# Kernel optimization log

Measured on AMD Instinct MI355X. Metric: run time of the kernel, lower is better.

The kernel has to match this reference:

```python
import jax, jax.numpy as jnp
import numpy as np

N = 300000   # nodes
E = 1500000  # edges
G = 30000    # graphs
R = 3        # relations
EMB = 32
HID = 64
OUT = 2


def rgcn_conv(x, src, dst, edge_type, W, root, bias, num_nodes):
    """PyG RGCNConv: out_i = x_i @ root + bias + sum_r mean_{j in N_r(i)} x_j @ W_r."""
    out = x @ root + bias
    for r in range(W.shape[0]):
        xr = x @ W[r]                                  # [N, out] transform once per relation
        mask = (edge_type == r).astype(x.dtype)        # [E]
        msg = xr[src] * mask[:, None]                  # gather + mask  [E, out]
        agg = jax.ops.segment_sum(msg, dst, num_segments=num_nodes)
        cnt = jax.ops.segment_sum(mask, dst, num_segments=num_nodes)
        out = out + agg / jnp.maximum(cnt, 1.0)[:, None]
    return out


def global_mean_pool(x, batch, num_graphs):
    s = jax.ops.segment_sum(x, batch, num_segments=num_graphs)
    c = jax.ops.segment_sum(jnp.ones((x.shape[0],), x.dtype), batch, num_segments=num_graphs)
    return s / jnp.maximum(c, 1.0)[:, None]


def setup_inputs() -> dict:
    key = jax.random.key(0)
    ks = jax.random.split(key, 16)
    def glorot(k, shape):
        fan_in, fan_out = shape[-2], shape[-1]
        lim = np.sqrt(6.0 / (fan_in + fan_out)).astype(np.float32)
        return jax.random.uniform(k, shape, jnp.float32, -lim, lim)
    return {
        "sid": jax.random.randint(ks[0], (N,), 0, 26),
        "cid": jax.random.randint(ks[1], (N,), 0, 10),
        "pid": jax.random.randint(ks[2], (N,), 0, 128),
        "edge_index": jax.random.randint(ks[3], (2, E), 0, N),
        "edge_type": jax.random.randint(ks[4], (E,), 0, R),
        "batch": jnp.sort(jax.random.randint(ks[5], (N,), 0, G)),
        "num_graphs": G,
        "shape_emb": jax.random.normal(ks[6], (26, EMB), jnp.float32),
        "col_emb": jax.random.normal(ks[7], (10, EMB), jnp.float32),
        "pos_emb": jax.random.normal(ks[8], (128, EMB), jnp.float32),
        "W1": glorot(ks[9], (R, EMB, HID)),
        "root1": glorot(ks[10], (EMB, HID)),
        "b1": jnp.zeros((HID,), jnp.float32),
        "W2": glorot(ks[11], (R, HID, HID)),
        "root2": glorot(ks[12], (HID, HID)),
        "b2": jnp.zeros((HID,), jnp.float32),
        "lin_W": glorot(ks[13], (HID, OUT)),
        "lin_b": jnp.zeros((OUT,), jnp.float32),
    }


def reference(sid, cid, pid, edge_index, edge_type, batch, num_graphs,
              shape_emb, col_emb, pos_emb,
              W1, root1, b1, W2, root2, b2, lin_W, lin_b):
    num_nodes = sid.shape[0]
    src, dst = edge_index[0], edge_index[1]
    x = shape_emb[sid] + col_emb[cid] + pos_emb[pid]          # [N, 32]
    x = jax.nn.relu(rgcn_conv(x, src, dst, edge_type, W1, root1, b1, num_nodes))
    x = jax.nn.relu(rgcn_conv(x, src, dst, edge_type, W2, root2, b2, num_nodes))
    g = global_mean_pool(x, batch, num_graphs)                 # [G, 64]
    return g @ lin_W + lin_b                                   # [G, 2]
```

## Files before the change

### kernel.cpp

```cpp
#include <hip/hip_runtime.h>
#include <hip/hip_bf16.h>

#define NREL 3
#define EMB 32
#define HID 64

typedef __attribute__((ext_vector_type(8))) short short8_t;
typedef __attribute__((ext_vector_type(4))) short short4_t;
typedef __attribute__((ext_vector_type(4))) float f32x4;

__device__ inline short f2bf(float v) {
  __hip_bfloat16 b = __float2bfloat16(v);
  short s;
  __builtin_memcpy(&s, &b, 2);
  return s;
}
__device__ inline float bf2f(short s) {
  __hip_bfloat16 b;
  __builtin_memcpy(&b, &s, 2);
  return __bfloat162float(b);
}
__device__ inline void split8(const float* v, short8_t* h, short8_t* l) {
#pragma unroll
  for (int i = 0; i < 8; i++) {
    short hh = f2bf(v[i]);
    (*h)[i] = hh;
    (*l)[i] = f2bf(v[i] - bf2f(hh));
  }
}

__global__ __launch_bounds__(256) void prep_k(
    const int* __restrict__ sid, const int* __restrict__ cid, const int* __restrict__ pid,
    const float* __restrict__ se, const float* __restrict__ ce, const float* __restrict__ pe,
    short* __restrict__ xh, short* __restrict__ xl,
    const int* __restrict__ dst, const int* __restrict__ et, int* __restrict__ icnt,
    const float* __restrict__ root1, const float* __restrict__ W1,
    const float* __restrict__ root2, const float* __restrict__ W2,
    short* __restrict__ w1h, short* __restrict__ w1l,
    short* __restrict__ w2h, short* __restrict__ w2l, int N, int E) {
  int i = blockIdx.x * 256 + threadIdx.x;
  if (i < N * 8) {
    int n = i >> 3, cg = i & 7;
    const float4 a = *(const float4*)&se[sid[n] * EMB + cg * 4];
    const float4 b = *(const float4*)&ce[cid[n] * EMB + cg * 4];
    const float4 c = *(const float4*)&pe[pid[n] * EMB + cg * 4];
    float v[4];
    v[0] = a.x + b.x + c.x; v[1] = a.y + b.y + c.y;
    v[2] = a.z + b.z + c.z; v[3] = a.w + b.w + c.w;
    short4_t h, l;
#pragma unroll
    for (int j = 0; j < 4; j++) {
      short hh = f2bf(v[j]);
      h[j] = hh;
      l[j] = f2bf(v[j] - bf2f(hh));
    }
    *(short4_t*)&xh[(size_t)n * EMB + cg * 4] = h;
    *(short4_t*)&xl[(size_t)n * EMB + cg * 4] = l;
  }
  if (i < E) atomicAdd(&icnt[et[i] * N + dst[i]], 1);
  if (i < 64 * 128) {
    int k = i >> 6, n = i & 63;
    float v = (k < EMB) ? root1[k * 64 + n] : W1[(k - EMB) * 64 + n];
    short h = f2bf(v);
    w1h[n * 128 + k] = h;
    w1l[n * 128 + k] = f2bf(v - bf2f(h));
  }
  if (i < 64 * 256) {
    int k = i >> 6, n = i & 63;
    float v = (k < HID) ? root2[k * 64 + n] : W2[(k - HID) * 64 + n];
    short h = f2bf(v);
    w2h[n * 256 + k] = h;
    w2l[n * 256 + k] = f2bf(v - bf2f(h));
  }
}

__global__ __launch_bounds__(256) void scan1_k(const int* __restrict__ icnt,
                                               int* __restrict__ psum, int M) {
  int base = blockIdx.x * 1024 + threadIdx.x * 4;
  int s = 0;
#pragma unroll
  for (int j = 0; j < 4; j++) {
    int i = base + j;
    if (i < M) s += icnt[i];
  }
  __shared__ int tmp[256];
  tmp[threadIdx.x] = s;
  __syncthreads();
  for (int off = 128; off > 0; off >>= 1) {
    if (threadIdx.x < off) tmp[threadIdx.x] += tmp[threadIdx.x + off];
    __syncthreads();
  }
  if (threadIdx.x == 0) psum[blockIdx.x] = tmp[0];
}

__global__ __launch_bounds__(256) void scan2_k(int* __restrict__ psum, int P) {
  __shared__ int tmp[256];
  __shared__ int carry_s;
  if (threadIdx.x == 0) carry_s = 0;
  __syncthreads();
  for (int base = 0; base < P; base += 256) {
    int i = base + threadIdx.x;
    int v = (i < P) ? psum[i] : 0;
    tmp[threadIdx.x] = v;
    __syncthreads();
    for (int off = 1; off < 256; off <<= 1) {
      int u = (threadIdx.x >= off) ? tmp[threadIdx.x - off] : 0;
      __syncthreads();
      tmp[threadIdx.x] += u;
      __syncthreads();
    }
    int carry = carry_s;
    if (i < P) psum[i] = carry + tmp[threadIdx.x] - v;
    __syncthreads();
    if (threadIdx.x == 0) carry_s = carry + tmp[255];
    __syncthreads();
  }
}

__global__ __launch_bounds__(256) void scan3_k(const int* __restrict__ icnt,
                                               const int* __restrict__ psum,
                                               int* __restrict__ offs, int M) {
  int base = blockIdx.x * 1024 + threadIdx.x * 4;
  int v[4];
  int s = 0;
#pragma unroll
  for (int j = 0; j < 4; j++) {
    int i = base + j;
    v[j] = (i < M) ? icnt[i] : 0;
    s += v[j];
  }
  __shared__ int tmp[256];
  tmp[threadIdx.x] = s;
  __syncthreads();
  for (int off = 1; off < 256; off <<= 1) {
    int u = (threadIdx.x >= off) ? tmp[threadIdx.x - off] : 0;
    __syncthreads();
    tmp[threadIdx.x] += u;
    __syncthreads();
  }
  int run = psum[blockIdx.x] + tmp[threadIdx.x] - s;
#pragma unroll
  for (int j = 0; j < 4; j++) {
    int i = base + j;
    if (i < M) {
      offs[i] = run;
      run += v[j];
    }
  }
}

__global__ __launch_bounds__(256) void scatter_k(const int* __restrict__ src,
                                                 const int* __restrict__ dst,
                                                 const int* __restrict__ et,
                                                 const int* __restrict__ offs,
                                                 int* __restrict__ cursor,
                                                 int* __restrict__ nbr,
                                                 int* __restrict__ csr, int E, int N) {
  int e = blockIdx.x * 256 + threadIdx.x;
  if (e >= E) return;
  int idx = et[e] * N + dst[e];
  int j = atomicAdd(&cursor[idx], 1);
  int s = src[e];
  if (j < 4) nbr[(size_t)idx * 4 + j] = s;
  else csr[offs[idx] + j] = s;
}

__global__ __launch_bounds__(256) void l1fused_k(
    const short* __restrict__ xh, const short* __restrict__ xl,
    const int* __restrict__ offs, const int* __restrict__ icnt,
    const int* __restrict__ nbr, const int* __restrict__ csr,
    const short* __restrict__ wth, const short* __restrict__ wtl,
    const float* __restrict__ bias, short* __restrict__ h1h, short* __restrict__ h1l, int N) {
  __shared__ __align__(16) short lws[64][16][8];
  __shared__ __align__(16) short gh_s[192][4][8];
  __shared__ __align__(16) short gl_s[192][4][8];
  __shared__ __align__(16) int4 mid_s[192];
  __shared__ int mlen_s[192];
  __shared__ int mbeg_s[192];

  const int t = threadIdx.x;
  const int lane = t & 63, w = t >> 6;
  const int m_ = lane & 15, q = lane >> 4;
  const int n0b = blockIdx.x * 64;

  int node_c = n0b + w * 16 + m_;
  if (node_c >= N) node_c = N - 1;
  short8_t ah0 = *(const short8_t*)&xh[(size_t)node_c * EMB + q * 8];
  short8_t al0 = *(const short8_t*)&xl[(size_t)node_c * EMB + q * 8];
#pragma unroll
  for (int i = 0; i < 4; i++) {
    int chi = t + 256 * i;
    int row = chi >> 4, c = chi & 15;
    short8_t wv = *(const short8_t*)&wth[(size_t)row * 128 + c * 8];
    *(short8_t*)&lws[row][c ^ (row & 7)][0] = wv;
  }
  if (t < 192) {
    int r = t >> 6, nl = t & 63;
    int n_ = n0b + nl;
    if (n_ >= N) n_ = N - 1;
    int idx = r * N + n_;
    mid_s[t] = *(const int4*)&nbr[(size_t)idx * 4];
    mlen_s[t] = icnt[idx];
    mbeg_s[t] = offs[idx];
  }
  __syncthreads();

  {
    int tslot[3], tq[3], tlen[3], tbeg[3];
    int4 tid4[3];
#pragma unroll
    for (int k = 0; k < 3; k++) {
      int tau = t + 256 * k;
      tslot[k] = tau >> 2;
      tq[k] = tau & 3;
      tid4[k] = mid_s[tslot[k]];
      tlen[k] = mlen_s[tslot[k]];
      tbeg[k] = mbeg_s[tslot[k]];
    }
    short8_t v0[3], v1[3], v2[3], v3[3];
#pragma unroll
    for (int k = 0; k < 3; k++) {
      int nself = n0b + (tslot[k] & 63);
      if (nself >= N) nself = N - 1;
      int g0 = (0 < tlen[k]) ? tid4[k].x : nself;
      int g1 = (1 < tlen[k]) ? tid4[k].y : nself;
      int g2 = (2 < tlen[k]) ? tid4[k].z : nself;
      int g3 = (3 < tlen[k]) ? tid4[k].w : nself;
      size_t co = (size_t)tq[k] * 8;
      v0[k] = *(const short8_t*)&xh[(size_t)g0 * EMB + co];
      v1[k] = *(const short8_t*)&xh[(size_t)g1 * EMB + co];
      v2[k] = *(const short8_t*)&xh[(size_t)g2 * EMB + co];
      v3[k] = *(const short8_t*)&xh[(size_t)g3 * EMB + co];
    }
#pragma unroll
    for (int k = 0; k < 3; k++) {
      float a[8];
      float k0 = (0 < tlen[k]) ? 1.f : 0.f;
      float k1 = (1 < tlen[k]) ? 1.f : 0.f;
      float k2 = (2 < tlen[k]) ? 1.f : 0.f;
      float k3 = (3 < tlen[k]) ? 1.f : 0.f;
#pragma unroll
      for (int i = 0; i < 8; i++)
        a[i] = k0 * bf2f(v0[k][i]) + k1 * bf2f(v1[k][i]) + k2 * bf2f(v2[k][i]) +
               k3 * bf2f(v3[k][i]);
      for (int j = 4; j < tlen[k]; j++) {
        short8_t u = *(const short8_t*)&xh[(size_t)csr[tbeg[k] + j] * EMB + tq[k] * 8];
#pragma unroll
        for (int i = 0; i < 8; i++) a[i] += bf2f(u[i]);
      }
      float inv = 1.f / fmaxf((float)tlen[k], 1.f);
#pragma unroll
      for (int i = 0; i < 8; i++) a[i] *= inv;
      short8_t hi, lo;
      split8(a, &hi, &lo);
      int qs = tq[k] ^ (tslot[k] & 3);
      *(short8_t*)&gh_s[tslot[k]][qs][0] = hi;
      *(short8_t*)&gl_s[tslot[k]][qs][0] = lo;
    }
  }
  __syncthreads();

  f32x4 acc[4];
#pragma unroll
  for (int i = 0; i < 4; i++) acc[i] = (f32x4){0.f, 0.f, 0.f, 0.f};
  short8_t ahv[4], alv[4];
#pragma unroll
  for (int g = 0; g < 4; g++) {
    if (g == 0) {
      ahv[0] = ah0;
      alv[0] = al0;
    } else {
      int slot = (g - 1) * 64 + w * 16 + m_;
      int qs = q ^ (slot & 3);
      ahv[g] = *(const short8_t*)&gh_s[slot][qs][0];
      alv[g] = *(const short8_t*)&gl_s[slot][qs][0];
    }
#pragma unroll
    for (int tt = 0; tt < 4; tt++) {
      int row = 16 * tt + m_;
      int cs = (g * 4 + q) ^ (row & 7);
      short8_t bh = *(const short8_t*)&lws[row][cs][0];
      acc[tt] = __builtin_amdgcn_mfma_f32_16x16x32_bf16(ahv[g], bh, acc[tt], 0, 0, 0);
      acc[tt] = __builtin_amdgcn_mfma_f32_16x16x32_bf16(alv[g], bh, acc[tt], 0, 0, 0);
    }
  }
  __syncthreads();

#pragma unroll
  for (int i = 0; i < 4; i++) {
    int chi = t + 256 * i;
    int row = chi >> 4, c = chi & 15;
    short8_t wv = *(const short8_t*)&wtl[(size_t)row * 128 + c * 8];
    *(short8_t*)&lws[row][c ^ (row & 7)][0] = wv;
  }
  __syncthreads();

#pragma unroll
  for (int g = 0; g < 4; g++) {
#pragma unroll
    for (int tt = 0; tt < 4; tt++) {
      int row = 16 * tt + m_;
      int cs = (g * 4 + q) ^ (row & 7);
      short8_t bl = *(const short8_t*)&lws[row][cs][0];
      acc[tt] = __builtin_amdgcn_mfma_f32_16x16x32_bf16(ahv[g], bl, acc[tt], 0, 0, 0);
    }
  }
#pragma unroll
  for (int tt = 0; tt < 4; tt++) {
    float bia = bias[16 * tt + m_];
#pragma unroll
    for (int reg = 0; reg < 4; reg++) {
      int node = n0b + w * 16 + q * 4 + reg;
      if (node < N) {
        float val = fmaxf(acc[tt][reg] + bia, 0.f);
        short hh = f2bf(val);
        h1h[(size_t)node * HID + 16 * tt + m_] = hh;
        h1l[(size_t)node * HID + 16 * tt + m_] = f2bf(val - bf2f(hh));
      }
    }
  }
}

__global__ __launch_bounds__(256) void l2fused_k(
    const short* __restrict__ h1h, const short* __restrict__ h1l,
    const int* __restrict__ offs, const int* __restrict__ icnt,
    const int* __restrict__ nbr, const int* __restrict__ csr,
    const short* __restrict__ wth, const short* __restrict__ wtl,
    const float* __restrict__ bias, const float* __restrict__ linW,
    const int* __restrict__ batch, float* __restrict__ gs, float* __restrict__ gc, int N) {
  __shared__ __align__(16) short lws[64][16][8];
  __shared__ __align__(16) short gh_s[192][4][8];
  __shared__ __align__(16) short gl_s[192][4][8];
  __shared__ __align__(16) int4 mid_s[192];
  __shared__ int mlen_s[192];
  __shared__ int mbeg_s[192];

  const int t = threadIdx.x;
  const int lane = t & 63, w = t >> 6;
  const int m_ = lane & 15, q = lane >> 4;
  const int n0b = blockIdx.x * 64;

  int node_c = n0b + w * 16 + m_;
  if (node_c >= N) node_c = N - 1;
  short8_t ash[2], asl[2];
#pragma unroll
  for (int s_ = 0; s_ < 2; s_++) {
    ash[s_] = *(const short8_t*)&h1h[(size_t)node_c * HID + s_ * 32 + q * 8];
    asl[s_] = *(const short8_t*)&h1l[(size_t)node_c * HID + s_ * 32 + q * 8];
  }
#pragma unroll
  for (int i = 0; i < 4; i++) {
    int chi = t + 256 * i;
    int row = chi >> 4, c = chi & 15;
    int g = c >> 2, qq = c & 3;
    short8_t wv = *(const short8_t*)&wth[(size_t)row * 256 + g * 64 + 0 * 32 + qq * 8];
    *(short8_t*)&lws[row][c ^ (row & 7)][0] = wv;
  }
  if (t < 192) {
    int r = t >> 6, nl = t & 63;
    int n_ = n0b + nl;
    if (n_ >= N) n_ = N - 1;
    int idx = r * N + n_;
    mid_s[t] = *(const int4*)&nbr[(size_t)idx * 4];
    mlen_s[t] = icnt[idx];
    mbeg_s[t] = offs[idx];
  }
  __syncthreads();

  f32x4 acc[4];
#pragma unroll
  for (int i = 0; i < 4; i++) acc[i] = (f32x4){0.f, 0.f, 0.f, 0.f};

#pragma unroll
  for (int s_ = 0; s_ < 2; s_++) {
    if (s_ == 1) {
#pragma unroll
      for (int i = 0; i < 4; i++) {
        int chi = t + 256 * i;
        int row = chi >> 4, c = chi & 15;
        int g = c >> 2, qq = c & 3;
        short8_t wv = *(const short8_t*)&wth[(size_t)row * 256 + g * 64 + 32 + qq * 8];
        *(short8_t*)&lws[row][c ^ (row & 7)][0] = wv;
      }
    }
    int tslot[3], tq[3], tlen[3], tbeg[3];
    int4 tid4[3];
#pragma unroll
    for (int k = 0; k < 3; k++) {
      int tau = t + 256 * k;
      tslot[k] = tau >> 2;
      tq[k] = tau & 3;
      tid4[k] = mid_s[tslot[k]];
      tlen[k] = mlen_s[tslot[k]];
      tbeg[k] = mbeg_s[tslot[k]];
    }
    short8_t v0[3], v1[3], v2[3], v3[3];
#pragma unroll
    for (int k = 0; k < 3; k++) {
      int nself = n0b + (tslot[k] & 63);
      if (nself >= N) nself = N - 1;
      int g0 = (0 < tlen[k]) ? tid4[k].x : nself;
      int g1 = (1 < tlen[k]) ? tid4[k].y : nself;
      int g2 = (2 < tlen[k]) ? tid4[k].z : nself;
      int g3 = (3 < tlen[k]) ? tid4[k].w : nself;
      size_t co = (size_t)s_ * 32 + tq[k] * 8;
      v0[k] = *(const short8_t*)&h1h[(size_t)g0 * HID + co];
      v1[k] = *(const short8_t*)&h1h[(size_t)g1 * HID + co];
      v2[k] = *(const short8_t*)&h1h[(size_t)g2 * HID + co];
      v3[k] = *(const short8_t*)&h1h[(size_t)g3 * HID + co];
    }
#pragma unroll
    for (int k = 0; k < 3; k++) {
      float a[8];
      float k0 = (0 < tlen[k]) ? 1.f : 0.f;
      float k1 = (1 < tlen[k]) ? 1.f : 0.f;
      float k2 = (2 < tlen[k]) ? 1.f : 0.f;
      float k3 = (3 < tlen[k]) ? 1.f : 0.f;
#pragma unroll
      for (int i = 0; i < 8; i++)
        a[i] = k0 * bf2f(v0[k][i]) + k1 * bf2f(v1[k][i]) + k2 * bf2f(v2[k][i]) +
               k3 * bf2f(v3[k][i]);
      for (int j = 4; j < tlen[k]; j++) {
        short8_t u =
            *(const short8_t*)&h1h[(size_t)csr[tbeg[k] + j] * HID + s_ * 32 + tq[k] * 8];
#pragma unroll
        for (int i = 0; i < 8; i++) a[i] += bf2f(u[i]);
      }
      float inv = 1.f / fmaxf((float)tlen[k], 1.f);
#pragma unroll
      for (int i = 0; i < 8; i++) a[i] *= inv;
      short8_t hi, lo;
      split8(a, &hi, &lo);
      int qs = tq[k] ^ (tslot[k] & 3);
      *(short8_t*)&gh_s[tslot[k]][qs][0] = hi;
      *(short8_t*)&gl_s[tslot[k]][qs][0] = lo;
    }
    __syncthreads();

    short8_t ahv[4], alv[4];
#pragma unroll
    for (int g = 0; g < 4; g++) {
      if (g == 0) {
        ahv[0] = ash[s_];
        alv[0] = asl[s_];
      } else {
        int slot = (g - 1) * 64 + w * 16 + m_;
        int qs = q ^ (slot & 3);
        ahv[g] = *(const short8_t*)&gh_s[slot][qs][0];
        alv[g] = *(const short8_t*)&gl_s[slot][qs][0];
      }
#pragma unroll
      for (int tt = 0; tt < 4; tt++) {
        int row = 16 * tt + m_;
        int cs = (g * 4 + q) ^ (row & 7);
        short8_t bh = *(const short8_t*)&lws[row][cs][0];
        acc[tt] = __builtin_amdgcn_mfma_f32_16x16x32_bf16(ahv[g], bh, acc[tt], 0, 0, 0);
        acc[tt] = __builtin_amdgcn_mfma_f32_16x16x32_bf16(alv[g], bh, acc[tt], 0, 0, 0);
      }
    }
    __syncthreads();

#pragma unroll
    for (int i = 0; i < 4; i++) {
      int chi = t + 256 * i;
      int row = chi >> 4, c = chi & 15;
      int g = c >> 2, qq = c & 3;
      short8_t wv = *(const short8_t*)&wtl[(size_t)row * 256 + g * 64 + s_ * 32 + qq * 8];
      *(short8_t*)&lws[row][c ^ (row & 7)][0] = wv;
    }
    __syncthreads();

#pragma unroll
    for (int g = 0; g < 4; g++) {
#pragma unroll
      for (int tt = 0; tt < 4; tt++) {
        int row = 16 * tt + m_;
        int cs = (g * 4 + q) ^ (row & 7);
        short8_t bl = *(const short8_t*)&lws[row][cs][0];
        acc[tt] = __builtin_amdgcn_mfma_f32_16x16x32_bf16(ahv[g], bl, acc[tt], 0, 0, 0);
      }
    }
    if (s_ == 0) __syncthreads();
  }

  float bia[4], lw0[4], lw1[4];
#pragma unroll
  for (int tt = 0; tt < 4; tt++) {
    int col = 16 * tt + m_;
    bia[tt] = bias[col];
    lw0[tt] = linW[col * 2 + 0];
    lw1[tt] = linW[col * 2 + 1];
  }
#pragma unroll
  for (int reg = 0; reg < 4; reg++) {
    int node = n0b + w * 16 + q * 4 + reg;
    float p0 = 0.f, p1 = 0.f;
#pragma unroll
    for (int tt = 0; tt < 4; tt++) {
      float v = fmaxf(acc[tt][reg] + bia[tt], 0.f);
      p0 += v * lw0[tt];
      p1 += v * lw1[tt];
    }
#pragma unroll
    for (int o = 1; o < 16; o <<= 1) {
      p0 += __shfl_xor(p0, o, 64);
      p1 += __shfl_xor(p1, o, 64);
    }
    if (m_ == 0 && node < N) {
      int g = batch[node];
      atomicAdd(&gs[g * 2 + 0], p0);
      atomicAdd(&gs[g * 2 + 1], p1);
      atomicAdd(&gc[g], 1.0f);
    }
  }
}

__global__ __launch_bounds__(256) void final_k(const float* __restrict__ gs,
                                               const float* __restrict__ gc,
                                               const float* __restrict__ linb,
                                               float* __restrict__ out, int G) {
  int i = blockIdx.x * 256 + threadIdx.x;
  if (i >= G * 2) return;
  int g = i >> 1, o = i & 1;
  out[i] = gs[i] / fmaxf(gc[g], 1.0f) + linb[o];
}

extern "C" void kernel_launch(void* const* d_in, const int* in_sizes, int n_in,
                              void* d_out, int out_size, void* d_ws, size_t ws_size,
                              hipStream_t stream) {
  const int* sid = (const int*)d_in[0];
  const int* cid = (const int*)d_in[1];
  const int* pid = (const int*)d_in[2];
  const int* ei = (const int*)d_in[3];
  const int* et = (const int*)d_in[4];
  const int* batch = (const int*)d_in[5];
  const float* se = (const float*)d_in[7];
  const float* ce = (const float*)d_in[8];
  const float* pe = (const float*)d_in[9];
  const float* W1 = (const float*)d_in[10];
  const float* root1 = (const float*)d_in[11];
  const float* b1 = (const float*)d_in[12];
  const float* W2 = (const float*)d_in[13];
  const float* root2 = (const float*)d_in[14];
  const float* b2 = (const float*)d_in[15];
  const float* linW = (const float*)d_in[16];
  const float* linb = (const float*)d_in[17];
  float* out = (float*)d_out;

  const int N = in_sizes[0];
  const int E = in_sizes[4];
  const int G = out_size / 2;
  const int* src = ei;
  const int* dst = ei + E;
  const int M = N * NREL;
  const int P = (M + 1023) / 1024;

  char* w = (char*)d_ws;
  short* h1h = (short*)w;  w += (size_t)N * HID * sizeof(short);
  short* h1l = (short*)w;  w += (size_t)N * HID * sizeof(short);
  short* xh = (short*)w;   w += (size_t)N * EMB * sizeof(short);
  short* xl = (short*)w;   w += (size_t)N * EMB * sizeof(short);
  float* gs = (float*)w;   w += (size_t)G * 2 * sizeof(float);
  float* gc = (float*)w;   w += (size_t)G * sizeof(float);
  int* icnt = (int*)w;     w += (size_t)M * sizeof(int);
  int* cursor = (int*)w;   w += (size_t)M * sizeof(int);
  int* offs = (int*)w;     w += (size_t)M * sizeof(int);
  int* nbr = (int*)w;      w += (size_t)M * 4 * sizeof(int);
  int* csr = (int*)w;      w += (size_t)E * sizeof(int);
  short* w1h = (short*)w;  w += (size_t)64 * 128 * sizeof(short);
  short* w1l = (short*)w;  w += (size_t)64 * 128 * sizeof(short);
  short* w2h = (short*)w;  w += (size_t)64 * 256 * sizeof(short);
  short* w2l = (short*)w;  w += (size_t)64 * 256 * sizeof(short);
  int* psum = (int*)w;     w += (size_t)P * sizeof(int);
  if ((size_t)(w - (char*)d_ws) > ws_size) return;

  hipMemsetAsync(icnt, 0, (size_t)2 * M * sizeof(int), stream);
  hipMemsetAsync(gs, 0, (size_t)G * 3 * sizeof(float), stream);

  int prep_n = N * 8;
  if (prep_n < E) prep_n = E;
  if (prep_n < 64 * 256) prep_n = 64 * 256;
  prep_k<<<(prep_n + 255) / 256, 256, 0, stream>>>(sid, cid, pid, se, ce, pe, xh, xl, dst, et,
                                                   icnt, root1, W1, root2, W2, w1h, w1l, w2h,
                                                   w2l, N, E);
  scan1_k<<<P, 256, 0, stream>>>(icnt, psum, M);
  scan2_k<<<1, 256, 0, stream>>>(psum, P);
  scan3_k<<<P, 256, 0, stream>>>(icnt, psum, offs, M);
  scatter_k<<<(E + 255) / 256, 256, 0, stream>>>(src, dst, et, offs, cursor, nbr, csr, E, N);

  int blocks = (N + 63) / 64;
  l1fused_k<<<blocks, 256, 0, stream>>>(xh, xl, offs, icnt, nbr, csr, w1h, w1l, b1, h1h, h1l,
                                        N);
  l2fused_k<<<blocks, 256, 0, stream>>>(h1h, h1l, offs, icnt, nbr, csr, w2h, w2l, b2, linW,
                                        batch, gs, gc, N);
  final_k<<<(G * 2 + 255) / 256, 256, 0, stream>>>(gs, gc, linb, out, G);
}
```

Baseline: 468.3 us.

## Replace per-(relation,node) CSR with per-block bucketed packed edge lists

Edges are now bucketed by destination block of 64 nodes, with dst-local index, relation and source packed into one 32-bit word. This replaces the three-pass per-(relation,node) scan, the cursor array and the inline-4 neighbour layout with a single small scan over block counts. The fused layer kernels then scatter-add gathered features into shared-memory fp32 accumulators using LDS atomics, and divide by counts before the MFMA stage. This cuts preprocessing memory traffic and kernel launches and balances edge work across threads, at the cost of many shared-memory float atomics and a 19-bit limit on source node ids.

```diff
diff --git a/kernel.cpp b/kernel.cpp
--- a/kernel.cpp
+++ b/kernel.cpp
@@ -33,7 +33,7 @@
     const int* __restrict__ sid, const int* __restrict__ cid, const int* __restrict__ pid,
     const float* __restrict__ se, const float* __restrict__ ce, const float* __restrict__ pe,
     short* __restrict__ xh, short* __restrict__ xl,
-    const int* __restrict__ dst, const int* __restrict__ et, int* __restrict__ icnt,
+    const int* __restrict__ dst, int* __restrict__ bcnt,
     const float* __restrict__ root1, const float* __restrict__ W1,
     const float* __restrict__ root2, const float* __restrict__ W2,
     short* __restrict__ w1h, short* __restrict__ w1l,
@@ -57,7 +57,7 @@
     *(short4_t*)&xh[(size_t)n * EMB + cg * 4] = h;
     *(short4_t*)&xl[(size_t)n * EMB + cg * 4] = l;
   }
-  if (i < E) atomicAdd(&icnt[et[i] * N + dst[i]], 1);
+  if (i < E) atomicAdd(&bcnt[dst[i] >> 6], 1);
   if (i < 64 * 128) {
     int k = i >> 6, n = i & 63;
     float v = (k < EMB) ? root1[k * 64 + n] : W1[(k - EMB) * 64 + n];
@@ -74,33 +74,16 @@
   }
 }
 
-__global__ __launch_bounds__(256) void scan1_k(const int* __restrict__ icnt,
-                                               int* __restrict__ psum, int M) {
-  int base = blockIdx.x * 1024 + threadIdx.x * 4;
-  int s = 0;
-#pragma unroll
-  for (int j = 0; j < 4; j++) {
-    int i = base + j;
-    if (i < M) s += icnt[i];
-  }
-  __shared__ int tmp[256];
-  tmp[threadIdx.x] = s;
-  __syncthreads();
-  for (int off = 128; off > 0; off >>= 1) {
-    if (threadIdx.x < off) tmp[threadIdx.x] += tmp[threadIdx.x + off];
-    __syncthreads();
-  }
-  if (threadIdx.x == 0) psum[blockIdx.x] = tmp[0];
-}
-
-__global__ __launch_bounds__(256) void scan2_k(int* __restrict__ psum, int P) {
+__global__ __launch_bounds__(256) void bscan_k(const int* __restrict__ bcnt,
+                                               int* __restrict__ boffs,
+                                               int* __restrict__ bcur, int NBk) {
   __shared__ int tmp[256];
   __shared__ int carry_s;
   if (threadIdx.x == 0) carry_s = 0;
   __syncthreads();
-  for (int base = 0; base < P; base += 256) {
+  for (int base = 0; base < NBk; base += 256) {
     int i = base + threadIdx.x;
-    int v = (i < P) ? psum[i] : 0;
+    int v = (i < NBk) ? bcnt[i] : 0;
     tmp[threadIdx.x] = v;
     __syncthreads();
     for (int off = 1; off < 256; off <<= 1) {
@@ -110,73 +93,38 @@
       __syncthreads();
     }
     int carry = carry_s;
-    if (i < P) psum[i] = carry + tmp[threadIdx.x] - v;
+    if (i < NBk) {
+      int ex = carry + tmp[threadIdx.x] - v;
+      boffs[i] = ex;
+      bcur[i] = ex;
+    }
     __syncthreads();
     if (threadIdx.x == 0) carry_s = carry + tmp[255];
     __syncthreads();
   }
-}
-
-__global__ __launch_bounds__(256) void scan3_k(const int* __restrict__ icnt,
-                                               const int* __restrict__ psum,
-                                               int* __restrict__ offs, int M) {
-  int base = blockIdx.x * 1024 + threadIdx.x * 4;
-  int v[4];
-  int s = 0;
-#pragma unroll
-  for (int j = 0; j < 4; j++) {
-    int i = base + j;
-    v[j] = (i < M) ? icnt[i] : 0;
-    s += v[j];
-  }
-  __shared__ int tmp[256];
-  tmp[threadIdx.x] = s;
-  __syncthreads();
-  for (int off = 1; off < 256; off <<= 1) {
-    int u = (threadIdx.x >= off) ? tmp[threadIdx.x - off] : 0;
-    __syncthreads();
-    tmp[threadIdx.x] += u;
-    __syncthreads();
-  }
-  int run = psum[blockIdx.x] + tmp[threadIdx.x] - s;
-#pragma unroll
-  for (int j = 0; j < 4; j++) {
-    int i = base + j;
-    if (i < M) {
-      offs[i] = run;
-      run += v[j];
-    }
-  }
-}
-
-__global__ __launch_bounds__(256) void scatter_k(const int* __restrict__ src,
-                                                 const int* __restrict__ dst,
-                                                 const int* __restrict__ et,
-                                                 const int* __restrict__ offs,
-                                                 int* __restrict__ cursor,
-                                                 int* __restrict__ nbr,
-                                                 int* __restrict__ csr, int E, int N) {
+  if (threadIdx.x == 0) boffs[NBk] = carry_s;
+}
+
+__global__ __launch_bounds__(256) void bscatter_k(const int* __restrict__ src,
+                                                  const int* __restrict__ dst,
+                                                  const int* __restrict__ et,
+                                                  int* __restrict__ bcur,
+                                                  unsigned* __restrict__ pk, int E) {
   int e = blockIdx.x * 256 + threadIdx.x;
   if (e >= E) return;
-  int idx = et[e] * N + dst[e];
-  int j = atomicAdd(&cursor[idx], 1);
-  int s = src[e];
-  if (j < 4) nbr[(size_t)idx * 4 + j] = s;
-  else csr[offs[idx] + j] = s;
+  int d = dst[e];
+  int pos = atomicAdd(&bcur[d >> 6], 1);
+  pk[pos] = ((unsigned)(d & 63) << 21) | ((unsigned)et[e] << 19) | (unsigned)src[e];
 }
 
 __global__ __launch_bounds__(256) void l1fused_k(
     const short* __restrict__ xh, const short* __restrict__ xl,
-    const int* __restrict__ offs, const int* __restrict__ icnt,
-    const int* __restrict__ nbr, const int* __restrict__ csr,
+    const int* __restrict__ boffs, const unsigned* __restrict__ pk,
     const short* __restrict__ wth, const short* __restrict__ wtl,
     const float* __restrict__ bias, short* __restrict__ h1h, short* __restrict__ h1l, int N) {
   __shared__ __align__(16) short lws[64][16][8];
-  __shared__ __align__(16) short gh_s[192][4][8];
-  __shared__ __align__(16) short gl_s[192][4][8];
-  __shared__ __align__(16) int4 mid_s[192];
-  __shared__ int mlen_s[192];
-  __shared__ int mbeg_s[192];
+  __shared__ float acc_s[192][33];
+  __shared__ int cnt_s[192];
 
   const int t = threadIdx.x;
   const int lane = t & 63, w = t >> 6;
@@ -194,68 +142,21 @@
     short8_t wv = *(const short8_t*)&wth[(size_t)row * 128 + c * 8];
     *(short8_t*)&lws[row][c ^ (row & 7)][0] = wv;
   }
-  if (t < 192) {
-    int r = t >> 6, nl = t & 63;
-    int n_ = n0b + nl;
-    if (n_ >= N) n_ = N - 1;
-    int idx = r * N + n_;
-    mid_s[t] = *(const int4*)&nbr[(size_t)idx * 4];
-    mlen_s[t] = icnt[idx];
-    mbeg_s[t] = offs[idx];
-  }
+  for (int i = t; i < 192 * 33; i += 256) ((float*)acc_s)[i] = 0.f;
+  if (t < 192) cnt_s[t] = 0;
   __syncthreads();
 
   {
-    int tslot[3], tq[3], tlen[3], tbeg[3];
-    int4 tid4[3];
-#pragma unroll
-    for (int k = 0; k < 3; k++) {
-      int tau = t + 256 * k;
-      tslot[k] = tau >> 2;
-      tq[k] = tau & 3;
-      tid4[k] = mid_s[tslot[k]];
-      tlen[k] = mlen_s[tslot[k]];
-      tbeg[k] = mbeg_s[tslot[k]];
-    }
-    short8_t v0[3], v1[3], v2[3], v3[3];
-#pragma unroll
-    for (int k = 0; k < 3; k++) {
-      int nself = n0b + (tslot[k] & 63);
-      if (nself >= N) nself = N - 1;
-      int g0 = (0 < tlen[k]) ? tid4[k].x : nself;
-      int g1 = (1 < tlen[k]) ? tid4[k].y : nself;
-      int g2 = (2 < tlen[k]) ? tid4[k].z : nself;
-      int g3 = (3 < tlen[k]) ? tid4[k].w : nself;
-      size_t co = (size_t)tq[k] * 8;
-      v0[k] = *(const short8_t*)&xh[(size_t)g0 * EMB + co];
-      v1[k] = *(const short8_t*)&xh[(size_t)g1 * EMB + co];
-      v2[k] = *(const short8_t*)&xh[(size_t)g2 * EMB + co];
-      v3[k] = *(const short8_t*)&xh[(size_t)g3 * EMB + co];
-    }
-#pragma unroll
-    for (int k = 0; k < 3; k++) {
-      float a[8];
-      float k0 = (0 < tlen[k]) ? 1.f : 0.f;
-      float k1 = (1 < tlen[k]) ? 1.f : 0.f;
-      float k2 = (2 < tlen[k]) ? 1.f : 0.f;
-      float k3 = (3 < tlen[k]) ? 1.f : 0.f;
-#pragma unroll
-      for (int i = 0; i < 8; i++)
-        a[i] = k0 * bf2f(v0[k][i]) + k1 * bf2f(v1[k][i]) + k2 * bf2f(v2[k][i]) +
-               k3 * bf2f(v3[k][i]);
-      for (int j = 4; j < tlen[k]; j++) {
-        short8_t u = *(const short8_t*)&xh[(size_t)csr[tbeg[k] + j] * EMB + tq[k] * 8];
-#pragma unroll
-        for (int i = 0; i < 8; i++) a[i] += bf2f(u[i]);
-      }
-      float inv = 1.f / fmaxf((float)tlen[k], 1.f);
-#pragma unroll
-      for (int i = 0; i < 8; i++) a[i] *= inv;
-      short8_t hi, lo;
-      split8(a, &hi, &lo);
-      int qs = tq[k] ^ (tslot[k] & 3);
-      *(short8_t*)&gh_s[tslot[k]][qs][0] = hi;
-      *(short8_t*)&gl_s[tslot[k]][qs][0] = lo;
+    int beg = boffs[blockIdx.x], end = boffs[blockIdx.x + 1];
+    const int qq = t & 3;
+    for (int e = beg + (t >> 2); e < end; e += 64) {
+      unsigned p = pk[e];
+      int srcn = p & 0x7FFFF;
+      int slot = ((p >> 19) & 3) * 64 + (int)(p >> 21);
+      short8_t v = *(const short8_t*)&xh[(size_t)srcn * EMB + qq * 8];
+#pragma unroll
+      for (int i = 0; i < 8; i++) atomicAdd(&acc_s[slot][qq * 8 + i], bf2f(v[i]));
+      if (qq == 0) atomicAdd(&cnt_s[slot], 1);
     }
   }
   __syncthreads();
@@ -271,9 +172,11 @@
       alv[0] = al0;
     } else {
       int slot = (g - 1) * 64 + w * 16 + m_;
-      int qs = q ^ (slot & 3);
-      ahv[g] = *(const short8_t*)&gh_s[slot][qs][0];
-      alv[g] = *(const short8_t*)&gl_s[slot][qs][0];
+      float inv = 1.f / fmaxf((float)cnt_s[slot], 1.f);
+      float a[8];
+#pragma unroll
+      for (int i = 0; i < 8; i++) a[i] = acc_s[slot][q * 8 + i] * inv;
+      split8(a, &ahv[g], &alv[g]);
     }
 #pragma unroll
     for (int tt = 0; tt < 4; tt++) {
@@ -323,17 +226,13 @@
 
 __global__ __launch_bounds__(256) void l2fused_k(
     const short* __restrict__ h1h, const short* __restrict__ h1l,
-    const int* __restrict__ offs, const int* __restrict__ icnt,
-    const int* __restrict__ nbr, const int* __restrict__ csr,
+    const int* __restrict__ boffs, const unsigned* __restrict__ pk,
     const short* __restrict__ wth, const short* __restrict__ wtl,
     const float* __restrict__ bias, const float* __restrict__ linW,
     const int* __restrict__ batch, float* __restrict__ gs, float* __restrict__ gc, int N) {
   __shared__ __align__(16) short lws[64][16][8];
-  __shared__ __align__(16) short gh_s[192][4][8];
-  __shared__ __align__(16) short gl_s[192][4][8];
-  __shared__ __align__(16) int4 mid_s[192];
-  __shared__ int mlen_s[192];
-  __shared__ int mbeg_s[192];
+  __shared__ float acc_s[192][33];
+  __shared__ int cnt_s[192];
 
   const int t = threadIdx.x;
   const int lane = t & 63, w = t >> 6;
@@ -356,84 +255,40 @@
     short8_t wv = *(const short8_t*)&wth[(size_t)row * 256 + g * 64 + 0 * 32 + qq * 8];
     *(short8_t*)&lws[row][c ^ (row & 7)][0] = wv;
   }
-  if (t < 192) {
-    int r = t >> 6, nl = t & 63;
-    int n_ = n0b + nl;
-    if (n_ >= N) n_ = N - 1;
-    int idx = r * N + n_;
-    mid_s[t] = *(const int4*)&nbr[(size_t)idx * 4];
-    mlen_s[t] = icnt[idx];
-    mbeg_s[t] = offs[idx];
-  }
+  for (int i = t; i < 192 * 33; i += 256) ((float*)acc_s)[i] = 0.f;
+  if (t < 192) cnt_s[t] = 0;
   __syncthreads();
 
   f32x4 acc[4];
 #pragma unroll
   for (int i = 0; i < 4; i++) acc[i] = (f32x4){0.f, 0.f, 0.f, 0.f};
+
+  const int beg = boffs[blockIdx.x], end = boffs[blockIdx.x + 1];
+  const int qq = t & 3;
 
 #pragma unroll
   for (int s_ = 0; s_ < 2; s_++) {
     if (s_ == 1) {
+      for (int i = t; i < 192 * 33; i += 256) ((float*)acc_s)[i] = 0.f;
+      if (t < 192) cnt_s[t] = 0;
 #pragma unroll
       for (int i = 0; i < 4; i++) {
         int chi = t + 256 * i;
         int row = chi >> 4, c = chi & 15;
-        int g = c >> 2, qq = c & 3;
-        short8_t wv = *(const short8_t*)&wth[(size_t)row * 256 + g * 64 + 32 + qq * 8];
+        int g = c >> 2, q2 = c & 3;
+        short8_t wv = *(const short8_t*)&wth[(size_t)row * 256 + g * 64 + 32 + q2 * 8];
         *(short8_t*)&lws[row][c ^ (row & 7)][0] = wv;
       }
-    }
-    int tslot[3], tq[3], tlen[3], tbeg[3];
-    int4 tid4[3];
-#pragma unroll
-    for (int k = 0; k < 3; k++) {
-      int tau = t + 256 * k;
-      tslot[k] = tau >> 2;
-      tq[k] = tau & 3;
-      tid4[k] = mid_s[tslot[k]];
-      tlen[k] = mlen_s[tslot[k]];
-      tbeg[k] = mbeg_s[tslot[k]];
-    }
-    short8_t v0[3], v1[3], v2[3], v3[3];
-#pragma unroll
-    for (int k = 0; k < 3; k++) {
-      int nself = n0b + (tslot[k] & 63);
-      if (nself >= N) nself = N - 1;
-      int g0 = (0 < tlen[k]) ? tid4[k].x : nself;
-      int g1 = (1 < tlen[k]) ? tid4[k].y : nself;
-      int g2 = (2 < tlen[k]) ? tid4[k].z : nself;
-      int g3 = (3 < tlen[k]) ? tid4[k].w : nself;
-      size_t co = (size_t)s_ * 32 + tq[k] * 8;
-      v0[k] = *(const short8_t*)&h1h[(size_t)g0 * HID + co];
-      v1[k] = *(const short8_t*)&h1h[(size_t)g1 * HID + co];
-      v2[k] = *(const short8_t*)&h1h[(size_t)g2 * HID + co];
-      v3[k] = *(const short8_t*)&h1h[(size_t)g3 * HID + co];
-    }
-#pragma unroll
-    for (int k = 0; k < 3; k++) {
-      float a[8];
-      float k0 = (0 < tlen[k]) ? 1.f : 0.f;
-      float k1 = (1 < tlen[k]) ? 1.f : 0.f;
-      float k2 = (2 < tlen[k]) ? 1.f : 0.f;
-      float k3 = (3 < tlen[k]) ? 1.f : 0.f;
-#pragma unroll
-      for (int i = 0; i < 8; i++)
-        a[i] = k0 * bf2f(v0[k][i]) + k1 * bf2f(v1[k][i]) + k2 * bf2f(v2[k][i]) +
-               k3 * bf2f(v3[k][i]);
-      for (int j = 4; j < tlen[k]; j++) {
-        short8_t u =
-            *(const short8_t*)&h1h[(size_t)csr[tbeg[k] + j] * HID + s_ * 32 + tq[k] * 8];
-#pragma unroll
-        for (int i = 0; i < 8; i++) a[i] += bf2f(u[i]);
-      }
-      float inv = 1.f / fmaxf((float)tlen[k], 1.f);
-#pragma unroll
-      for (int i = 0; i < 8; i++) a[i] *= inv;
-      short8_t hi, lo;
-      split8(a, &hi, &lo);
-      int qs = tq[k] ^ (tslot[k] & 3);
-      *(short8_t*)&gh_s[tslot[k]][qs][0] = hi;
-      *(short8_t*)&gl_s[tslot[k]][qs][0] = lo;
+      __syncthreads();
+    }
+    for (int e = beg + (t >> 2); e < end; e += 64) {
+      unsigned p = pk[e];
+      int srcn = p & 0x7FFFF;
+      int slot = ((p >> 19) & 3) * 64 + (int)(p >> 21);
+      short8_t v = *(const short8_t*)&h1h[(size_t)srcn * HID + s_ * 32 + qq * 8];
+#pragma unroll
+      for (int i = 0; i < 8; i++) atomicAdd(&acc_s[slot][qq * 8 + i], bf2f(v[i]));
+      if (qq == 0) atomicAdd(&cnt_s[slot], 1);
     }
     __syncthreads();
 
@@ -445,9 +300,11 @@
         alv[0] = asl[s_];
       } else {
         int slot = (g - 1) * 64 + w * 16 + m_;
-        int qs = q ^ (slot & 3);
-        ahv[g] = *(const short8_t*)&gh_s[slot][qs][0];
-        alv[g] = *(const short8_t*)&gl_s[slot][qs][0];
+        float inv = 1.f / fmaxf((float)cnt_s[slot], 1.f);
+        float a[8];
+#pragma unroll
+        for (int i = 0; i < 8; i++) a[i] = acc_s[slot][q * 8 + i] * inv;
+        split8(a, &ahv[g], &alv[g]);
       }
 #pragma unroll
       for (int tt = 0; tt < 4; tt++) {
@@ -464,8 +321,8 @@
     for (int i = 0; i < 4; i++) {
       int chi = t + 256 * i;
       int row = chi >> 4, c = chi & 15;
-      int g = c >> 2, qq = c & 3;
-      short8_t wv = *(const short8_t*)&wtl[(size_t)row * 256 + g * 64 + s_ * 32 + qq * 8];
+      int g = c >> 2, q2 = c & 3;
+      short8_t wv = *(const short8_t*)&wtl[(size_t)row * 256 + g * 64 + s_ * 32 + q2 * 8];
       *(short8_t*)&lws[row][c ^ (row & 7)][0] = wv;
     }
     __syncthreads();
@@ -552,8 +409,8 @@
   const int G = out_size / 2;
   const int* src = ei;
   const int* dst = ei + E;
-  const int M = N * NREL;
-  const int P = (M + 1023) / 1024;
+  const int NBk = (N + 63) / 64;
+  const int NBa = (NBk + 15) & ~15;
 
   char* w = (char*)d_ws;
   short* h1h = (short*)w;  w += (size_t)N * HID * sizeof(short);
@@ -562,36 +419,30 @@
   short* xl = (short*)w;   w += (size_t)N * EMB * sizeof(short);
   float* gs = (float*)w;   w += (size_t)G * 2 * sizeof(float);
   float* gc = (float*)w;   w += (size_t)G * sizeof(float);
-  int* icnt = (int*)w;     w += (size_t)M * sizeof(int);
-  int* cursor = (int*)w;   w += (size_t)M * sizeof(int);
-  int* offs = (int*)w;     w += (size_t)M * sizeof(int);
-  int* nbr = (int*)w;      w += (size_t)M * 4 * sizeof(int);
-  int* csr = (int*)w;      w += (size_t)E * sizeof(int);
+  int* bcnt = (int*)w;     w += (size_t)NBa * sizeof(int);
+  int* bcur = (int*)w;     w += (size_t)NBa * sizeof(int);
+  int* boffs = (int*)w;    w += (size_t)(NBa + 16) * sizeof(int);
+  unsigned* pk = (unsigned*)w; w += (size_t)E * sizeof(unsigned);
   short* w1h = (short*)w;  w += (size_t)64 * 128 * sizeof(short);
   short* w1l = (short*)w;  w += (size_t)64 * 128 * sizeof(short);
   short* w2h = (short*)w;  w += (size_t)64 * 256 * sizeof(short);
   short* w2l = (short*)w;  w += (size_t)64 * 256 * sizeof(short);
-  int* psum = (int*)w;     w += (size_t)P * sizeof(int);
   if ((size_t)(w - (char*)d_ws) > ws_size) return;
 
-  hipMemsetAsync(icnt, 0, (size_t)2 * M * sizeof(int), stream);
+  hipMemsetAsync(bcnt, 0, (size_t)NBa * sizeof(int), stream);
   hipMemsetAsync(gs, 0, (size_t)G * 3 * sizeof(float), stream);
 
   int prep_n = N * 8;
   if (prep_n < E) prep_n = E;
   if (prep_n < 64 * 256) prep_n = 64 * 256;
-  prep_k<<<(prep_n + 255) / 256, 256, 0, stream>>>(sid, cid, pid, se, ce, pe, xh, xl, dst, et,
-                                                   icnt, root1, W1, root2, W2, w1h, w1l, w2h,
+  prep_k<<<(prep_n + 255) / 256, 256, 0, stream>>>(sid, cid, pid, se, ce, pe, xh, xl, dst,
+                                                   bcnt, root1, W1, root2, W2, w1h, w1l, w2h,
                                                    w2l, N, E);
-  scan1_k<<<P, 256, 0, stream>>>(icnt, psum, M);
-  scan2_k<<<1, 256, 0, stream>>>(psum, P);
-  scan3_k<<<P, 256, 0, stream>>>(icnt, psum, offs, M);
-  scatter_k<<<(E + 255) / 256, 256, 0, stream>>>(src, dst, et, offs, cursor, nbr, csr, E, N);
-
-  int blocks = (N + 63) / 64;
-  l1fused_k<<<blocks, 256, 0, stream>>>(xh, xl, offs, icnt, nbr, csr, w1h, w1l, b1, h1h, h1l,
-                                        N);
-  l2fused_k<<<blocks, 256, 0, stream>>>(h1h, h1l, offs, icnt, nbr, csr, w2h, w2l, b2, linW,
-                                        batch, gs, gc, N);
+  bscan_k<<<1, 256, 0, stream>>>(bcnt, boffs, bcur, NBk);
+  bscatter_k<<<(E + 255) / 256, 256, 0, stream>>>(src, dst, et, bcur, pk, E);
+
+  l1fused_k<<<NBk, 256, 0, stream>>>(xh, xl, boffs, pk, w1h, w1l, b1, h1h, h1l, N);
+  l2fused_k<<<NBk, 256, 0, stream>>>(h1h, h1l, boffs, pk, w2h, w2l, b2, linW, batch, gs, gc,
+                                     N);
   final_k<<<(G * 2 + 255) / 256, 256, 0, stream>>>(gs, gc, linb, out, G);
 }
```

Result: slower. 1.139 ms (+143.3%).
